# Kernel tuning notes

Hardware: AMD Instinct MI355X
Metric: run time of the kernel (lower is better)

## Reference

```python
import jax, jax.numpy as jnp
import numpy as np

L, T, F = 16, 1 << 19, 2
N_MIN, N_MAX = 16, 2048
N_POINTS = 1 << 21
_PRIMES = (np.uint32(1), np.uint32(2654435761))


def _resolutions(L, N_min, N_max):
    if L == 1:
        return [N_min]
    b = (N_max / N_min) ** (1.0 / (L - 1))
    return [int(round(N_min * b ** l)) for l in range(L)]


def _hash(cx, cy, table_size):
    # XOR of coord_i * prime_i, mod T. T is a power of two, so uint32
    # wraparound matches torch's int64 arithmetic in the low bits.
    h = cx.astype(jnp.uint32) * _PRIMES[0]
    h = h ^ (cy.astype(jnp.uint32) * _PRIMES[1])
    return (h % jnp.uint32(table_size)).astype(jnp.int32)


def setup_inputs() -> dict:
    key = jax.random.key(0)
    k1, k2 = jax.random.split(key)
    xy = jax.random.uniform(k1, (N_POINTS, 2), dtype=jnp.float32)
    # matches torch.empty(T,F).uniform_(-1e-4, 1e-4) per level
    tables = (jax.random.uniform(k2, (L, T, F), dtype=jnp.float32) * 2.0 - 1.0) * 1e-4
    return {"xy": xy, "tables": tables}


def reference(xy, tables):
    # xy: (P, 2) in [0,1]; tables: (L, T, F). Returns (P, L*F).
    res = _resolutions(L, N_MIN, N_MAX)
    feats = []
    for l in range(L):
        N = res[l]
        scaled = xy * N                      # (P, 2)
        i0 = jnp.floor(scaled).astype(jnp.int32)
        t = scaled - i0.astype(xy.dtype)
        wx, wy = t[..., 0:1], t[..., 1:2]    # (P, 1)
        corners = []
        for dy in (0, 1):
            for dx in (0, 1):
                cx = (i0[..., 0] + dx) % N
                cy = (i0[..., 1] + dy) % N
                h = _hash(cx, cy, T)         # (P,)
                corners.append(tables[l][h]) # (P, F)
        c00, c10, c01, c11 = corners
        f0 = c00 * (1 - wx) + c10 * wx
        f1 = c01 * (1 - wx) + c11 * wx
        feats.append(f0 * (1 - wy) + f1 * wy)
    return jnp.concatenate(feats, axis=-1)   # (P, L*F)
```

## Files before the change

### kernel.cpp

```cpp
#include <hip/hip_runtime.h>
#include <math.h>

#define NPOINTS (1 << 21)
#define LVL 16
#define TSIZE (1 << 19)
#define TMASK (TSIZE - 1)
#define PRIME2 2654435761u

#define GBITS 9
#define GRES (1 << GBITS)
#define SCAN_CHUNK 1024
#define CB 1024
#define PPB 8192
#define NB1 (NPOINTS / PPB)
#define MSIZE (CB * NB1)
#define NCHUNKS (MSIZE / SCAN_CHUNK)
#define CAP 2560

typedef float f32x2 __attribute__((ext_vector_type(2)));
typedef float f32x4 __attribute__((ext_vector_type(4)));

struct Params {
    int   n[LVL];
    float fn[LVL];
};

__device__ __forceinline__ unsigned part1by1(unsigned v) {
    v &= 0xFFFFu;
    v = (v | (v << 8)) & 0x00FF00FFu;
    v = (v | (v << 4)) & 0x0F0F0F0Fu;
    v = (v | (v << 2)) & 0x33333333u;
    v = (v | (v << 1)) & 0x55555555u;
    return v;
}

__device__ __forceinline__ unsigned morton_key(f32x2 pt) {
    int kx = (int)(pt.x * (float)GRES);
    int ky = (int)(pt.y * (float)GRES);
    kx = min(max(kx, 0), GRES - 1);
    ky = min(max(ky, 0), GRES - 1);
    return (part1by1((unsigned)ky) << 1) | part1by1((unsigned)kx);
}

__device__ __forceinline__ f32x2 level_feat(const f32x2* __restrict__ tables,
                                            int l, int N, float fN, f32x2 pt)
{
    float sx = pt.x * fN;
    float sy = pt.y * fN;
    float fx = floorf(sx);
    float fy = floorf(sy);
    float wx = sx - fx;
    float wy = sy - fy;
    int ix = (int)fx;
    int iy = (int)fy;

    int cx0 = (ix     >= N) ? ix - N     : ix;
    int cx1 = (ix + 1 >= N) ? ix + 1 - N : ix + 1;
    int cy0 = (iy     >= N) ? iy - N     : iy;
    int cy1 = (iy + 1 >= N) ? iy + 1 - N : iy + 1;

    unsigned hy0 = (unsigned)cy0 * PRIME2;
    unsigned hy1 = (unsigned)cy1 * PRIME2;

    const f32x2* tbl = tables + (size_t)l * TSIZE;
    f32x2 c00 = tbl[(int)(((unsigned)cx0 ^ hy0) & TMASK)];
    f32x2 c10 = tbl[(int)(((unsigned)cx1 ^ hy0) & TMASK)];
    f32x2 c01 = tbl[(int)(((unsigned)cx0 ^ hy1) & TMASK)];
    f32x2 c11 = tbl[(int)(((unsigned)cx1 ^ hy1) & TMASK)];

    float omx = 1.0f - wx, omy = 1.0f - wy;
    float f0x = c00.x * omx + c10.x * wx;
    float f0y = c00.y * omx + c10.y * wx;
    float f1x = c01.x * omx + c11.x * wx;
    float f1y = c01.y * omx + c11.y * wx;

    f32x2 r;
    r.x = f0x * omy + f1x * wy;
    r.y = f0y * omy + f1y * wy;
    return r;
}

__global__ __launch_bounds__(256) void hist1_kernel(
    const f32x2* __restrict__ xy, unsigned* __restrict__ M)
{
    __shared__ unsigned lh[CB];
    int tid = threadIdx.x, b = blockIdx.x;
    for (int k = tid; k < CB; k += 256) lh[k] = 0;
    __syncthreads();
    int base = b * PPB;
    #pragma unroll
    for (int i = 0; i < PPB / 256; ++i) {
        f32x2 pt = __builtin_nontemporal_load(&xy[base + i * 256 + tid]);
        atomicAdd(&lh[morton_key(pt) >> 8], 1u);
    }
    __syncthreads();
    for (int k = tid; k < CB; k += 256) M[k * NB1 + b] = lh[k];
}

__global__ __launch_bounds__(SCAN_CHUNK) void scan_local_kernel(
    unsigned* __restrict__ hist, unsigned* __restrict__ aux)
{
    __shared__ unsigned s[SCAN_CHUNK];
    int t = threadIdx.x;
    int i = blockIdx.x * SCAN_CHUNK + t;
    unsigned v = hist[i];
    s[t] = v;
    __syncthreads();
    #pragma unroll
    for (int o = 1; o < SCAN_CHUNK; o <<= 1) {
        unsigned x = (t >= o) ? s[t - o] : 0u;
        __syncthreads();
        s[t] += x;
        __syncthreads();
    }
    hist[i] = s[t] - v;
    if (t == SCAN_CHUNK - 1) aux[blockIdx.x] = s[t];
}

__global__ __launch_bounds__(NCHUNKS) void scan_aux_kernel(unsigned* __restrict__ aux)
{
    __shared__ unsigned s[NCHUNKS];
    int t = threadIdx.x;
    unsigned v = aux[t];
    s[t] = v;
    __syncthreads();
    #pragma unroll
    for (int o = 1; o < NCHUNKS; o <<= 1) {
        unsigned x = (t >= o) ? s[t - o] : 0u;
        __syncthreads();
        s[t] += x;
        __syncthreads();
    }
    aux[t] = s[t] - v;
}

__global__ __launch_bounds__(256) void scatter1_kernel(
    const f32x2* __restrict__ xy, const unsigned* __restrict__ M,
    const unsigned* __restrict__ aux, f32x4* __restrict__ slotsA)
{
    __shared__ unsigned cur[CB];
    int tid = threadIdx.x, b = blockIdx.x;
    for (int k = tid; k < CB; k += 256) {
        unsigned idx = (unsigned)k * NB1 + b;
        cur[k] = M[idx] + aux[idx >> 10];
    }
    __syncthreads();
    int base = b * PPB;
    #pragma unroll
    for (int i = 0; i < PPB / 256; ++i) {
        int p = base + i * 256 + tid;
        f32x2 pt = __builtin_nontemporal_load(&xy[p]);
        unsigned k = morton_key(pt) >> 8;
        unsigned pos = atomicAdd(&cur[k], 1u);
        f32x4 s = { pt.x, pt.y, __uint_as_float((unsigned)p), 0.0f };
        slotsA[pos] = s;
    }
}

__global__ __launch_bounds__(256) void fine_kernel(
    const f32x4* __restrict__ slotsA, const unsigned* __restrict__ M,
    const unsigned* __restrict__ aux, f32x4* __restrict__ slotsB)
{
    __shared__ f32x4 buf[CAP];
    __shared__ unsigned fh[256];
    __shared__ unsigned fc[256];

    int tid = threadIdx.x;
    int k   = blockIdx.x;

    unsigned i0 = (unsigned)k * NB1;
    unsigned start = M[i0] + aux[i0 >> 10];
    unsigned end;
    if (k == CB - 1) end = NPOINTS;
    else {
        unsigned i1 = (unsigned)(k + 1) * NB1;
        end = M[i1] + aux[i1 >> 10];
    }
    unsigned n = end - start;
    unsigned m = n > CAP ? CAP : n;

    fh[tid] = 0;
    __syncthreads();
    for (unsigned i = tid; i < m; i += 256) {
        f32x4 s = slotsA[start + i];
        buf[i] = s;
        f32x2 pt = { s.x, s.y };
        atomicAdd(&fh[morton_key(pt) & 255u], 1u);
    }
    __syncthreads();
    unsigned v = fh[tid];
    fc[tid] = v;
    __syncthreads();
    #pragma unroll
    for (int o = 1; o < 256; o <<= 1) {
        unsigned x = (tid >= o) ? fc[tid - o] : 0u;
        __syncthreads();
        fc[tid] += x;
        __syncthreads();
    }
    unsigned excl = fc[tid] - v;
    __syncthreads();
    fc[tid] = excl;
    __syncthreads();
    for (unsigned i = tid; i < m; i += 256) {
        f32x4 s = buf[i];
        f32x2 pt = { s.x, s.y };
        unsigned r = atomicAdd(&fc[morton_key(pt) & 255u], 1u);
        slotsB[start + r] = s;
    }
    for (unsigned i = CAP + tid; i < n; i += 256)
        slotsB[start + i] = slotsA[start + i];
}

__global__ __launch_bounds__(256) void main_kernel(
    const f32x4* __restrict__ slots,
    const f32x2* __restrict__ tables,
    f32x4* __restrict__ out,
    Params P)
{
    int bid = (blockIdx.x & 7) * 1024 + (blockIdx.x >> 3);
    int sp  = bid * 256 + threadIdx.x;
    f32x4 s = __builtin_nontemporal_load(&slots[sp]);
    f32x2 pt = { s.x, s.y };
    unsigned op = __float_as_uint(s.z);
    f32x4* o = out + (size_t)op * 8;

    f32x2 r[8];
    #pragma unroll
    for (int j = 0; j < 8; ++j)
        r[j] = level_feat(tables, j, P.n[j], P.fn[j], pt);
    #pragma unroll
    for (int q = 0; q < 4; ++q) {
        f32x4 v = { r[2 * q].x, r[2 * q].y, r[2 * q + 1].x, r[2 * q + 1].y };
        o[q] = v;
    }
    #pragma unroll
    for (int j = 0; j < 8; ++j)
        r[j] = level_feat(tables, 8 + j, P.n[8 + j], P.fn[8 + j], pt);
    #pragma unroll
    for (int q = 0; q < 4; ++q) {
        f32x4 v = { r[2 * q].x, r[2 * q].y, r[2 * q + 1].x, r[2 * q + 1].y };
        o[4 + q] = v;
    }
}

__global__ __launch_bounds__(256, 6) void hashgrid2d_fallback(
    const f32x2* __restrict__ xy,
    const f32x2* __restrict__ tables,
    f32x4* __restrict__ out,
    Params P)
{
    __shared__ f32x4 lds[256 * 5];

    int tid = threadIdx.x;
    int p   = blockIdx.x * 256 + tid;

    f32x2 pt = __builtin_nontemporal_load(&xy[p]);
    size_t base = (size_t)blockIdx.x * 2048;

    #pragma unroll
    for (int b = 0; b < 2; ++b) {
        #pragma unroll
        for (int q = 0; q < 4; ++q) {
            float f[4];
            #pragma unroll
            for (int j = 0; j < 2; ++j) {
                int l = b * 8 + q * 2 + j;
                f32x2 r = level_feat(tables, l, P.n[l], P.fn[l], pt);
                f[j * 2 + 0] = r.x;
                f[j * 2 + 1] = r.y;
            }
            f32x4 v = { f[0], f[1], f[2], f[3] };
            lds[tid * 5 + q] = v;
        }
        __syncthreads();
        #pragma unroll
        for (int i = 0; i < 4; ++i) {
            int e  = i * 256 + tid;
            int pp = e >> 2;
            int q  = e & 3;
            f32x4 v = lds[pp * 5 + q];
            __builtin_nontemporal_store(v, &out[base + pp * 8 + b * 4 + q]);
        }
        __syncthreads();
    }
}

extern "C" void kernel_launch(void* const* d_in, const int* in_sizes, int n_in,
                              void* d_out, int out_size, void* d_ws, size_t ws_size,
                              hipStream_t stream) {
    const f32x2* xy     = (const f32x2*)d_in[0];
    const f32x2* tables = (const f32x2*)d_in[1];
    f32x4* out = (f32x4*)d_out;

    Params P;
    double b = pow(2048.0 / 16.0, 1.0 / 15.0);
    for (int l = 0; l < LVL; ++l) {
        int N = (int)llround(16.0 * pow(b, (double)l));
        P.n[l]  = N;
        P.fn[l] = (float)N;
    }

    const size_t WS_NEED = 66u << 20;

    if (ws_size >= WS_NEED) {
        char* w = (char*)d_ws;
        unsigned* M      = (unsigned*)(w);
        unsigned* aux    = (unsigned*)(w + (1u << 20));
        f32x4*    slotsA = (f32x4*)   (w + (2u << 20));
        f32x4*    slotsB = (f32x4*)   (w + (34u << 20));

        hist1_kernel     <<<NB1,           256,        0, stream>>>(xy, M);
        scan_local_kernel<<<NCHUNKS,       SCAN_CHUNK, 0, stream>>>(M, aux);
        scan_aux_kernel  <<<1,             NCHUNKS,    0, stream>>>(aux);
        scatter1_kernel  <<<NB1,           256,        0, stream>>>(xy, M, aux, slotsA);
        fine_kernel      <<<CB,            256,        0, stream>>>(slotsA, M, aux, slotsB);
        main_kernel      <<<NPOINTS / 256, 256,        0, stream>>>(slotsB, tables, out, P);
    } else {
        hashgrid2d_fallback<<<NPOINTS / 256, 256, 0, stream>>>(xy, tables, out, P);
    }
}
```

Measured before the change: 263.9 us.

## Stage per-block bounding-box grid corners in LDS pool for hash lookups

Each block of Morton-sorted points computes its bounding box with shared-memory atomics, then for each level whose covering grid window fits in a 2560-entry LDS pool, cooperatively gathers the hashed table entries into LDS. Per-point interpolation then reads corners from LDS instead of scattered global gathers, falling back to the global hash lookup for levels that do not fit. This aims to cut redundant global gathers from neighbouring points. In exchange it adds three block barriers, atomics and a cooperative load phase, plus LDS use that may lower occupancy.

```diff
diff --git a/kernel.cpp b/kernel.cpp
--- a/kernel.cpp
+++ b/kernel.cpp
@@ -17,6 +17,8 @@
 #define NCHUNKS (MSIZE / SCAN_CHUNK)
 #define CAP 2560
 
+#define POOL 2560
+
 typedef float f32x2 __attribute__((ext_vector_type(2)));
 typedef float f32x4 __attribute__((ext_vector_type(4)));
 
@@ -80,6 +82,37 @@
     return r;
 }
 
+__device__ __forceinline__ f32x2 feat_any(
+    int l, int N, float fN, f32x2 pt,
+    const f32x2* pool, const int* s_m1, const int* s_m2,
+    const f32x2* __restrict__ tables)
+{
+    int m1 = s_m1[l];
+    if (m1 >= 0) {
+        int off = m1 & 0xFFFF, W = m1 >> 16;
+        int m2 = s_m2[l];
+        int ix0 = m2 & 0xFFFF, iy0 = m2 >> 16;
+        float sx = pt.x * fN, sy = pt.y * fN;
+        float fx = floorf(sx), fy = floorf(sy);
+        float wx = sx - fx,   wy = sy - fy;
+        int dx = (int)fx - ix0;
+        int dy = (int)fy - iy0;
+        int base = off + dy * W + dx;
+        f32x2 c00 = pool[base],     c10 = pool[base + 1];
+        f32x2 c01 = pool[base + W], c11 = pool[base + W + 1];
+        float omx = 1.0f - wx, omy = 1.0f - wy;
+        float f0x = c00.x * omx + c10.x * wx;
+        float f0y = c00.y * omx + c10.y * wx;
+        float f1x = c01.x * omx + c11.x * wx;
+        float f1y = c01.y * omx + c11.y * wx;
+        f32x2 r;
+        r.x = f0x * omy + f1x * wy;
+        r.y = f0y * omy + f1y * wy;
+        return r;
+    }
+    return level_feat(tables, l, N, fN, pt);
+}
+
 __global__ __launch_bounds__(256) void hist1_kernel(
     const f32x2* __restrict__ xy, unsigned* __restrict__ M)
 {
@@ -218,17 +251,79 @@
     f32x4* __restrict__ out,
     Params P)
 {
+    __shared__ f32x2 pool[POOL];
+    __shared__ int s_m1[LVL];
+    __shared__ int s_m2[LVL];
+    __shared__ int s_sz[LVL];
+    __shared__ unsigned bb[4];
+
+    int tid = threadIdx.x;
     int bid = (blockIdx.x & 7) * 1024 + (blockIdx.x >> 3);
-    int sp  = bid * 256 + threadIdx.x;
+    int sp  = bid * 256 + tid;
+
     f32x4 s = __builtin_nontemporal_load(&slots[sp]);
     f32x2 pt = { s.x, s.y };
     unsigned op = __float_as_uint(s.z);
+
+    if (tid < 4) bb[tid] = (tid & 1) ? 0u : 0xFFFFFFFFu;
+    __syncthreads();
+    unsigned ux = __float_as_uint(pt.x), uy = __float_as_uint(pt.y);
+    atomicMin(&bb[0], ux); atomicMax(&bb[1], ux);
+    atomicMin(&bb[2], uy); atomicMax(&bb[3], uy);
+    __syncthreads();
+
+    if (tid == 0) {
+        float xmin = __uint_as_float(bb[0]);
+        float xmax = __uint_as_float(bb[1]);
+        float ymin = __uint_as_float(bb[2]);
+        float ymax = __uint_as_float(bb[3]);
+        int off = 0;
+        for (int l = 0; l < LVL; ++l) {
+            float fN = P.fn[l];
+            int ix0 = (int)floorf(xmin * fN);
+            int ix1 = (int)floorf(xmax * fN);
+            int iy0 = (int)floorf(ymin * fN);
+            int iy1 = (int)floorf(ymax * fN);
+            int W = ix1 - ix0 + 2;
+            int H = iy1 - iy0 + 2;
+            int sz = W * H;
+            if (off + sz <= POOL) {
+                s_m1[l] = off | (W << 16);
+                s_m2[l] = ix0 | (iy0 << 16);
+                s_sz[l] = sz;
+                off += sz;
+            } else {
+                s_m1[l] = -1;
+            }
+        }
+    }
+    __syncthreads();
+
+    for (int l = 0; l < LVL; ++l) {
+        int m1 = s_m1[l];
+        if (m1 < 0) continue;
+        int off = m1 & 0xFFFF, W = m1 >> 16;
+        int m2 = s_m2[l];
+        int ix0 = m2 & 0xFFFF, iy0 = m2 >> 16;
+        int sz = s_sz[l];
+        int N  = P.n[l];
+        const f32x2* tbl = tables + (size_t)l * TSIZE;
+        for (int t = tid; t < sz; t += 256) {
+            int dy = t / W;
+            int dx = t - dy * W;
+            int cx = ix0 + dx; if (cx >= N) cx -= N;
+            int cy = iy0 + dy; if (cy >= N) cy -= N;
+            unsigned h = ((unsigned)cx ^ ((unsigned)cy * PRIME2)) & TMASK;
+            pool[off + t] = tbl[h];
+        }
+    }
+    __syncthreads();
+
     f32x4* o = out + (size_t)op * 8;
-
     f32x2 r[8];
     #pragma unroll
     for (int j = 0; j < 8; ++j)
-        r[j] = level_feat(tables, j, P.n[j], P.fn[j], pt);
+        r[j] = feat_any(j, P.n[j], P.fn[j], pt, pool, s_m1, s_m2, tables);
     #pragma unroll
     for (int q = 0; q < 4; ++q) {
         f32x4 v = { r[2 * q].x, r[2 * q].y, r[2 * q + 1].x, r[2 * q + 1].y };
@@ -236,7 +331,7 @@
     }
     #pragma unroll
     for (int j = 0; j < 8; ++j)
-        r[j] = level_feat(tables, 8 + j, P.n[8 + j], P.fn[8 + j], pt);
+        r[j] = feat_any(8 + j, P.n[8 + j], P.fn[8 + j], pt, pool, s_m1, s_m2, tables);
     #pragma unroll
     for (int q = 0; q < 4; ++q) {
         f32x4 v = { r[2 * q].x, r[2 * q].y, r[2 * q + 1].x, r[2 * q + 1].y };
```

Measured after the change: 288.4 us. 9.3% more time.
